# Performance work log

Measured on AMD Instinct MI355X. Metric: run time of the kernel, lower is better.

## Reference

```python
import jax, jax.numpy as jnp
import numpy as np
from jax import lax


def _pw(x, w, b):
    # pointwise conv1d (kernel_size=1) on [B,C,L]
    return jnp.einsum('oc,bcl->bol', w, x) + b[None, :, None]


def _conv(x, w, b, stride):
    y = lax.conv_general_dilated(x, w, (stride,), 'VALID',
                                 dimension_numbers=('NCH', 'OIH', 'NCH'))
    return y + b[None, :, None]


def setup_inputs() -> dict:
    key = jax.random.key(0)
    ks = jax.random.split(key, 40)
    B, L = 512, 300
    d = {}
    d['x'] = jax.random.randint(ks[0], (B, L), 0, 23)
    def w(k, shape, s=0.1):
        return jax.random.normal(k, shape, dtype=jnp.float32) * s
    d['emb'] = w(ks[1], (23, 128), 1.0)
    d['dr_w'] = w(ks[2], (64, 128)); d['dr_b'] = w(ks[3], (64,), 0.01)
    d['c1_w'] = w(ks[4], (64, 64)); d['c1_b'] = w(ks[5], (64,), 0.01)
    d['c11_w'] = w(ks[6], (64, 64)); d['c11_b'] = w(ks[7], (64,), 0.01)
    d['c12_w'] = w(ks[8], (64, 64)); d['c12_b'] = w(ks[9], (64,), 0.01)
    d['c21_w'] = w(ks[10], (64, 64)); d['c21_b'] = w(ks[11], (64,), 0.01)
    d['c22_w'] = w(ks[12], (64, 64)); d['c22_b'] = w(ks[13], (64,), 0.01)
    d['c31_w'] = w(ks[14], (64, 64)); d['c31_b'] = w(ks[15], (64,), 0.01)
    d['c32_w'] = w(ks[16], (64, 64)); d['c32_b'] = w(ks[17], (64,), 0.01)
    d['c41_w'] = w(ks[18], (64, 64)); d['c41_b'] = w(ks[19], (64,), 0.01)
    d['fc_w'] = w(ks[20], (64, 320)); d['fc_b'] = w(ks[21], (64,), 0.01)
    d['cp1_w'] = w(ks[22], (64, 64, 4)); d['cp1_b'] = w(ks[23], (64,), 0.01)
    d['cp2_w'] = w(ks[24], (64, 64, 5)); d['cp2_b'] = w(ks[25], (64,), 0.01)
    d['wt'] = w(ks[26], (64, 64)); d['wx'] = w(ks[27], (64, 64))
    d['bh'] = w(ks[28], (64,), 0.01)
    d['wa'] = w(ks[29], (64,)); d['ba'] = w(ks[30], (1,), 0.01)
    d['m1_w'] = w(ks[31], (100, 960)); d['m1_b'] = w(ks[32], (100,), 0.01)
    d['m2_w'] = w(ks[33], (1, 100)); d['m2_b'] = w(ks[34], (1,), 0.01)
    return d


def reference(x, emb, dr_w, dr_b, c1_w, c1_b, c11_w, c11_b, c12_w, c12_b,
              c21_w, c21_b, c22_w, c22_b, c31_w, c31_b, c32_w, c32_b,
              c41_w, c41_b, fc_w, fc_b, cp1_w, cp1_b, cp2_w, cp2_b,
              wt, wx, bh, wa, ba, m1_w, m1_b, m2_w, m2_b):
    h = emb[x]                                  # [B,L,128]
    h = jnp.transpose(h, (0, 2, 1))             # [B,128,L]
    r = _pw(h, dr_w, dr_b)                      # [B,64,L]
    r = _pw(r, c1_w, c1_b)
    x2 = _pw(_pw(r, c11_w, c11_b), c12_w, c12_b)
    x3 = _pw(_pw(r, c21_w, c21_b), c22_w, c22_b)
    x4 = _pw(_pw(r, c31_w, c31_b), c32_w, c32_b)
    # MaxPool1d(k=3, s=1, p=1)
    xp = jnp.pad(r, ((0, 0), (0, 0), (1, 1)), constant_values=-jnp.inf)
    p = jnp.maximum(jnp.maximum(xp[:, :, :-2], xp[:, :, 1:-1]), xp[:, :, 2:])
    x5 = _pw(p, c41_w, c41_b)
    h = jnp.concatenate([r, x2, x3, x4, x5], axis=1)   # [B,320,L]
    h = _pw(h, fc_w, fc_b)                             # [B,64,L]
    h = _conv(h, cp1_w, cp1_b, 4)                      # [B,64,75]
    a_in = jnp.transpose(h, (0, 2, 1))                 # [B,75,64]
    # additive attention emission
    qt = a_in @ wt.T                                   # Wt(inputs)
    kx = a_in @ wx.T                                   # Wx(inputs)
    hsc = jnp.tanh(qt[:, :, None, :] + kx[:, None, :, :] + bh)  # [B,75,75,64]
    e = jnp.einsum('bijd,d->bij', hsc, wa) + ba[0]     # [B,75,75]
    a = jax.nn.softmax(e, axis=-1)
    v = jnp.einsum('bij,bjd->bid', a, a_in)            # [B,75,64]
    h = jnp.transpose(v, (0, 2, 1))                    # [B,64,75]
    h = jax.nn.relu(h)
    h = _conv(h, cp2_w, cp2_b, 5)                      # [B,64,15]
    h = h.reshape(h.shape[0], -1)                      # [B,960]
    h = jax.nn.relu(h @ m1_w.T + m1_b)
    return h @ m2_w.T + m2_b                           # [B,1]
```

## Files before the change

kernel.cpp:

```cpp
#include <hip/hip_runtime.h>
#include <hip/hip_bf16.h>

#define DEV __device__ __forceinline__

DEV float fexp2(float x) {
#if __has_builtin(__builtin_amdgcn_exp2f)
  return __builtin_amdgcn_exp2f(x);
#else
  return exp2f(x);
#endif
}
DEV float frcp(float x) {
#if __has_builtin(__builtin_amdgcn_rcpf)
  return __builtin_amdgcn_rcpf(x);
#else
  return 1.0f / x;
#endif
}

#define K_C2LOG2E 2.8853900817779268f

__global__ void __launch_bounds__(256)
prep1(const float* __restrict__ emb,
      const float* __restrict__ dr_w, const float* __restrict__ dr_b,
      const float* __restrict__ c1_w, const float* __restrict__ c1_b,
      const float* __restrict__ w11, const float* __restrict__ b11,
      const float* __restrict__ w12, const float* __restrict__ b12,
      const float* __restrict__ w21, const float* __restrict__ b21,
      const float* __restrict__ w22, const float* __restrict__ b22,
      const float* __restrict__ w31, const float* __restrict__ b31,
      const float* __restrict__ w32, const float* __restrict__ b32,
      const float* __restrict__ fc_w, const float* __restrict__ fc_b,
      const float* __restrict__ c41_w, const float* __restrict__ c41_b,
      float* __restrict__ rt_ext, float* __restrict__ T4,
      float* __restrict__ W5, float* __restrict__ bias_fc)
{
  const int v = blockIdx.x, tid = threadIdx.x;
  if (v < 23) {
    __shared__ float A[64], Rt[64], X2[3][64];
    const int c = tid & 63;
    if (tid < 64) {
      float acc = dr_b[c];
      #pragma unroll 8
      for (int e = 0; e < 32; ++e) {
        const float4 wv = *(const float4*)&dr_w[c * 128 + 4 * e];
        const float4 ev = *(const float4*)&emb[v * 128 + 4 * e];
        acc = fmaf(wv.x, ev.x, acc); acc = fmaf(wv.y, ev.y, acc);
        acc = fmaf(wv.z, ev.z, acc); acc = fmaf(wv.w, ev.w, acc);
      }
      A[c] = acc;
    }
    __syncthreads();
    if (tid < 64) {
      float acc = c1_b[c];
      for (int m = 0; m < 64; ++m) acc = fmaf(c1_w[c * 64 + m], A[m], acc);
      Rt[c] = acc;
      rt_ext[v * 64 + c] = acc;
    }
    for (int br = 0; br < 3; ++br) {
      const float* w1 = (br == 0) ? w11 : (br == 1) ? w21 : w31;
      const float* b1 = (br == 0) ? b11 : (br == 1) ? b21 : b31;
      const float* w2 = (br == 0) ? w12 : (br == 1) ? w22 : w32;
      const float* b2 = (br == 0) ? b12 : (br == 1) ? b22 : b32;
      __syncthreads();
      if (tid < 64) {
        float acc = b1[c];
        for (int m = 0; m < 64; ++m) acc = fmaf(w1[c * 64 + m], Rt[m], acc);
        A[c] = acc;
      }
      __syncthreads();
      if (tid < 64) {
        float acc = b2[c];
        for (int m = 0; m < 64; ++m) acc = fmaf(w2[c * 64 + m], A[m], acc);
        X2[br][c] = acc;
      }
    }
    __syncthreads();
    if (tid < 64) {
      float acc = 0.f;
      for (int m = 0; m < 64; ++m) acc = fmaf(fc_w[c * 320 + m],       Rt[m],    acc);
      for (int m = 0; m < 64; ++m) acc = fmaf(fc_w[c * 320 + 64 + m],  X2[0][m], acc);
      for (int m = 0; m < 64; ++m) acc = fmaf(fc_w[c * 320 + 128 + m], X2[1][m], acc);
      for (int m = 0; m < 64; ++m) acc = fmaf(fc_w[c * 320 + 192 + m], X2[2][m], acc);
      T4[v * 64 + c] = acc;
    }
  } else {
    if (tid < 64) rt_ext[23 * 64 + tid] = -1e30f;
    const int m = tid & 63, c0 = (tid >> 6) * 16;
    float acc[16];
    #pragma unroll
    for (int r = 0; r < 16; ++r) acc[r] = 0.f;
    for (int q = 0; q < 64; ++q) {
      const float w = c41_w[q * 64 + m];
      #pragma unroll
      for (int r = 0; r < 16; ++r)
        acc[r] = fmaf(fc_w[(c0 + r) * 320 + 256 + q], w, acc[r]);
    }
    #pragma unroll
    for (int r = 0; r < 16; ++r) W5[(c0 + r) * 64 + m] = acc[r];
    if (tid < 64) {
      float a2 = fc_b[tid];
      for (int q = 0; q < 64; ++q) a2 = fmaf(fc_w[tid * 320 + 256 + q], c41_b[q], a2);
      bias_fc[tid] = a2;
    }
  }
}

__global__ void tab_T5G(const float* __restrict__ cp1_w, const float* __restrict__ cp1_b,
                        const float* __restrict__ T4, const float* __restrict__ W5,
                        const float* __restrict__ bias_fc,
                        float* __restrict__ T5, float* __restrict__ G, float* __restrict__ bb)
{
  const int idx = blockIdx.x * 256 + threadIdx.x;
  if (idx < 5888) {
    const int v = idx >> 8, r = idx & 255, k = r >> 6, o = r & 63;
    float acc = 0.f;
    for (int c = 0; c < 64; ++c) acc = fmaf(cp1_w[o * 256 + c * 4 + k], T4[v * 64 + c], acc);
    T5[v * 256 + k * 64 + o] = acc;
  } else if (idx < 5888 + 16384) {
    const int j = idx - 5888;
    const int k = j >> 12, m = (j >> 6) & 63, o = j & 63;
    float acc = 0.f;
    for (int c = 0; c < 64; ++c) acc = fmaf(cp1_w[o * 256 + c * 4 + k], W5[c * 64 + m], acc);
    G[k * 4096 + m * 64 + o] = acc;
  } else if (idx < 22336) {
    const int o = idx - 22272;
    float acc = cp1_b[o];
    for (int c = 0; c < 64; ++c) {
      float wsum = cp1_w[o * 256 + c * 4 + 0] + cp1_w[o * 256 + c * 4 + 1]
                 + cp1_w[o * 256 + c * 4 + 2] + cp1_w[o * 256 + c * 4 + 3];
      acc = fmaf(wsum, bias_fc[c], acc);
    }
    bb[o] = acc;
  }
}

__global__ void __launch_bounds__(256)
tab_FP5(const float* __restrict__ G, const float* __restrict__ rt_ext,
        float* __restrict__ FP5)
{
  __shared__ float Gl[2][64][64];
  __shared__ float rtl[24 * 64];
  const int tid = threadIdx.x, lane = tid & 63, wave = tid >> 6;
  const int h = blockIdx.x & 1;
  const int vbase = (blockIdx.x >> 1) * 32;
  for (int i = tid; i < 1536; i += 256) rtl[i] = rt_ext[i];
  for (int i = tid; i < 8192; i += 256) ((float*)Gl)[i] = G[h * 8192 + i];
  __syncthreads();
  for (int g = 0; g < 2; ++g) {
    const int j0 = vbase + wave * 8 + g * 4;
    float p[4];
    #pragma unroll
    for (int r = 0; r < 4; ++r) {
      const int v = j0 + r;
      const int a = v / 576, rem = v - a * 576, c = rem / 24, dd = rem - c * 24;
      p[r] = fmaxf(fmaxf(rtl[a * 64 + lane], rtl[c * 64 + lane]), rtl[dd * 64 + lane]);
    }
    float acc[4][2];
    #pragma unroll
    for (int r = 0; r < 4; ++r) { acc[r][0] = 0.f; acc[r][1] = 0.f; }
    #pragma unroll
    for (int m = 0; m < 64; ++m) {
      const float g0 = Gl[0][m][lane], g1 = Gl[1][m][lane];
      #pragma unroll
      for (int r = 0; r < 4; ++r) {
        const float pv = __shfl(p[r], m);
        acc[r][0] = fmaf(g0, pv, acc[r][0]);
        acc[r][1] = fmaf(g1, pv, acc[r][1]);
      }
    }
    #pragma unroll
    for (int r = 0; r < 4; ++r) {
      const int v = j0 + r;
      FP5[v * 256 + (2 * h + 0) * 64 + lane] = acc[r][0];
      FP5[v * 256 + (2 * h + 1) * 64 + lane] = acc[r][1];
    }
  }
}

__global__ void __launch_bounds__(512)
k_main(const int* __restrict__ x,
       const float* __restrict__ wt, const float* __restrict__ wx,
       const float* __restrict__ bh, const float* __restrict__ wa,
       const float* __restrict__ T5, const float* __restrict__ FP5,
       const float* __restrict__ bb, float* __restrict__ vv)
{
  __shared__ int x_lds[304];
  __shared__ __align__(16) float a_in_lds[75 * 64];
  __shared__ __align__(16) float qt_lds[75 * 68];
  __shared__ __align__(16) float kx_lds[75 * 65];
  __shared__ __align__(16) float tail_lds[75 * 12];
  __shared__ float wa_lds[64];

  const int tid = threadIdx.x, lane = tid & 63, wave = tid >> 6;
  const int b = blockIdx.x;

  for (int i = tid; i < 300; i += 512) x_lds[i] = x[b * 300 + i];
  if (tid < 64) wa_lds[tid] = wa[tid];
  __syncthreads();

  {
    const float bbv = bb[lane];
    for (int t = wave; t < 75; t += 8) {
      float acc = bbv;
      #pragma unroll
      for (int k = 0; k < 4; ++k) {
        const int l = 4 * t + k;
        const int xa = (l == 0) ? 23 : x_lds[l - 1];
        const int xd = (l == 299) ? 23 : x_lds[l + 1];
        const int trip = (xa * 576 + x_lds[l] * 24 + xd) * 256;
        acc += T5[x_lds[l] * 256 + k * 64 + lane];
        acc += FP5[trip + k * 64 + lane];
      }
      a_in_lds[t * 64 + lane] = acc;
    }
  }
  __syncthreads();

  {
    float qacc[10];
    #pragma unroll
    for (int r = 0; r < 10; ++r) qacc[r] = 0.f;
    for (int c = 0; c < 4; ++c) {
      const float4 w0 = *(const float4*)&wt[lane * 64 + 16 * c];
      const float4 w1 = *(const float4*)&wt[lane * 64 + 16 * c + 4];
      const float4 w2 = *(const float4*)&wt[lane * 64 + 16 * c + 8];
      const float4 w3 = *(const float4*)&wt[lane * 64 + 16 * c + 12];
      #pragma unroll
      for (int r = 0; r < 10; ++r) {
        const int i = wave + 8 * r;
        if (i < 75) {
          const float* arow = &a_in_lds[i * 64 + 16 * c];
          const float4 a0 = *(const float4*)&arow[0];
          const float4 a1 = *(const float4*)&arow[4];
          const float4 a2 = *(const float4*)&arow[8];
          const float4 a3 = *(const float4*)&arow[12];
          float acc = qacc[r];
          acc = fmaf(w0.x, a0.x, acc); acc = fmaf(w0.y, a0.y, acc);
          acc = fmaf(w0.z, a0.z, acc); acc = fmaf(w0.w, a0.w, acc);
          acc = fmaf(w1.x, a1.x, acc); acc = fmaf(w1.y, a1.y, acc);
          acc = fmaf(w1.z, a1.z, acc); acc = fmaf(w1.w, a1.w, acc);
          acc = fmaf(w2.x, a2.x, acc); acc = fmaf(w2.y, a2.y, acc);
          acc = fmaf(w2.z, a2.z, acc); acc = fmaf(w2.w, a2.w, acc);
          acc = fmaf(w3.x, a3.x, acc); acc = fmaf(w3.y, a3.y, acc);
          acc = fmaf(w3.z, a3.z, acc); acc = fmaf(w3.w, a3.w, acc);
          qacc[r] = acc;
        }
      }
    }
    const float bhv = bh[lane];
    #pragma unroll
    for (int r = 0; r < 10; ++r) {
      const int i = wave + 8 * r;
      if (i < 75) qt_lds[i * 68 + lane] = (qacc[r] + bhv) * K_C2LOG2E;
    }

    #pragma unroll
    for (int r = 0; r < 10; ++r) qacc[r] = 0.f;
    for (int c = 0; c < 4; ++c) {
      const float4 w0 = *(const float4*)&wx[lane * 64 + 16 * c];
      const float4 w1 = *(const float4*)&wx[lane * 64 + 16 * c + 4];
      const float4 w2 = *(const float4*)&wx[lane * 64 + 16 * c + 8];
      const float4 w3 = *(const float4*)&wx[lane * 64 + 16 * c + 12];
      #pragma unroll
      for (int r = 0; r < 10; ++r) {
        const int i = wave + 8 * r;
        if (i < 75) {
          const float* arow = &a_in_lds[i * 64 + 16 * c];
          const float4 a0 = *(const float4*)&arow[0];
          const float4 a1 = *(const float4*)&arow[4];
          const float4 a2 = *(const float4*)&arow[8];
          const float4 a3 = *(const float4*)&arow[12];
          float acc = qacc[r];
          acc = fmaf(w0.x, a0.x, acc); acc = fmaf(w0.y, a0.y, acc);
          acc = fmaf(w0.z, a0.z, acc); acc = fmaf(w0.w, a0.w, acc);
          acc = fmaf(w1.x, a1.x, acc); acc = fmaf(w1.y, a1.y, acc);
          acc = fmaf(w1.z, a1.z, acc); acc = fmaf(w1.w, a1.w, acc);
          acc = fmaf(w2.x, a2.x, acc); acc = fmaf(w2.y, a2.y, acc);
          acc = fmaf(w2.z, a2.z, acc); acc = fmaf(w2.w, a2.w, acc);
          acc = fmaf(w3.x, a3.x, acc); acc = fmaf(w3.y, a3.y, acc);
          acc = fmaf(w3.z, a3.z, acc); acc = fmaf(w3.w, a3.w, acc);
          qacc[r] = acc;
        }
      }
    }
    #pragma unroll
    for (int r = 0; r < 10; ++r) {
      const int i = wave + 8 * r;
      if (i < 75) kx_lds[i * 65 + lane] = qacc[r] * K_C2LOG2E;
    }
  }
  __syncthreads();

  for (int idx = tid; idx < 825; idx += 512) {
    const int i = idx / 11, jt = idx - i * 11;
    const float* qrow = &qt_lds[i * 68];
    const float* krow = &kx_lds[(64 + jt) * 65];
    float S = 0.f;
    #pragma unroll 8
    for (int dd = 0; dd < 64; ++dd) {
      const int d = (dd + lane) & 63;
      const float r = frcp(1.f + fexp2(qrow[d] + krow[d]));
      S = fmaf(wa_lds[d], r, S);
    }
    tail_lds[i * 12 + jt] = S;
  }
  __syncthreads();

  for (int i = wave; i < 75; i += 8) {
    const float* krow = &kx_lds[lane * 65];
    float S1 = 0.f;
    #pragma unroll
    for (int q = 0; q < 16; ++q) {
      const float4 q4 = *(const float4*)&qt_lds[i * 68 + 4 * q];
      const float4 w4 = *(const float4*)&wa_lds[4 * q];
      float r;
      r = frcp(1.f + fexp2(q4.x + krow[4 * q + 0])); S1 = fmaf(w4.x, r, S1);
      r = frcp(1.f + fexp2(q4.y + krow[4 * q + 1])); S1 = fmaf(w4.y, r, S1);
      r = frcp(1.f + fexp2(q4.z + krow[4 * q + 2])); S1 = fmaf(w4.z, r, S1);
      r = frcp(1.f + fexp2(q4.w + krow[4 * q + 3])); S1 = fmaf(w4.w, r, S1);
    }
    const float z1 = S1 * (-K_C2LOG2E);
    const float zt = (lane < 11) ? tail_lds[i * 12 + lane] * (-K_C2LOG2E) : -1e30f;
    float m = fmaxf(z1, zt);
    #pragma unroll
    for (int off = 32; off; off >>= 1) m = fmaxf(m, __shfl_xor(m, off));
    const float p1 = fexp2(z1 - m);
    const float p2 = (lane < 11) ? fexp2(zt - m) : 0.f;
    float s = p1 + p2;
    #pragma unroll
    for (int off = 32; off; off >>= 1) s += __shfl_xor(s, off);
    const float inv = frcp(s);
    const float a1 = p1 * inv, a2 = p2 * inv;

    float acc = 0.f;
    #pragma unroll
    for (int jj = 0; jj < 64; ++jj)
      acc = fmaf(__shfl(a1, jj), a_in_lds[jj * 64 + lane], acc);
    #pragma unroll
    for (int jj = 0; jj < 11; ++jj)
      acc = fmaf(__shfl(a2, jj), a_in_lds[(64 + jj) * 64 + lane], acc);
    vv[b * 4800 + i * 64 + lane] = fmaxf(acc, 0.f);
  }
}

__global__ void __launch_bounds__(256)
k_tail(const float* __restrict__ vv,
       const float* __restrict__ cp2_w, const float* __restrict__ cp2_b,
       const float* __restrict__ m1_w, const float* __restrict__ m1_b,
       const float* __restrict__ m2_w, const float* __restrict__ m2_b,
       float* __restrict__ out)
{
  __shared__ __align__(16) float vv_lds[75 * 65];
  __shared__ float g_lds[2][960];
  __shared__ float y_lds[2][100];
  const int tid = threadIdx.x, lane = tid & 63, wave = tid >> 6;
  const int b0 = blockIdx.x * 2;

  for (int q = 0; q < 2; ++q) {
    const int b = b0 + q;
    __syncthreads();
    for (int idx = tid; idx < 4800; idx += 256) {
      const int i = idx >> 6, d = idx & 63;
      vv_lds[i * 65 + d] = vv[b * 4800 + idx];
    }
    __syncthreads();
    for (int idx = tid; idx < 960; idx += 256) {
      const int o = idx / 15, s = idx % 15;
      float acc = cp2_b[o];
      for (int c = 0; c < 64; ++c) {
        const float* wrow = &cp2_w[(o * 64 + c) * 5];
        const float* vrow = &vv_lds[5 * s * 65 + c];
        #pragma unroll
        for (int k = 0; k < 5; ++k)
          acc = fmaf(wrow[k], vrow[k * 65], acc);
      }
      g_lds[q][idx] = acc;
    }
  }
  __syncthreads();

  for (int u = wave; u < 100; u += 4) {
    float acc0 = 0.f, acc1 = 0.f;
    #pragma unroll
    for (int it = 0; it < 15; ++it) {
      const int n = it * 64 + lane;
      const float w = m1_w[u * 960 + n];
      acc0 = fmaf(w, g_lds[0][n], acc0);
      acc1 = fmaf(w, g_lds[1][n], acc1);
    }
    #pragma unroll
    for (int off = 32; off; off >>= 1) {
      acc0 += __shfl_xor(acc0, off);
      acc1 += __shfl_xor(acc1, off);
    }
    if (lane == 0) {
      const float mb = m1_b[u];
      y_lds[0][u] = fmaxf(acc0 + mb, 0.f);
      y_lds[1][u] = fmaxf(acc1 + mb, 0.f);
    }
  }
  __syncthreads();
  if (wave < 2) {
    const int q = wave;
    float s = y_lds[q][lane] * m2_w[lane];
    if (lane < 36) s = fmaf(y_lds[q][lane + 64], m2_w[lane + 64], s);
    #pragma unroll
    for (int off = 32; off; off >>= 1) s += __shfl_xor(s, off);
    if (lane == 0) out[b0 + q] = s + m2_b[0];
  }
}

extern "C" void kernel_launch(void* const* d_in, const int* in_sizes, int n_in,
                              void* d_out, int out_size, void* d_ws, size_t ws_size,
                              hipStream_t stream) {
  (void)in_sizes; (void)n_in; (void)out_size; (void)ws_size;
  const int*   x     = (const int*)  d_in[0];
  const float* emb   = (const float*)d_in[1];
  const float* dr_w  = (const float*)d_in[2];
  const float* dr_b  = (const float*)d_in[3];
  const float* c1_w  = (const float*)d_in[4];
  const float* c1_b  = (const float*)d_in[5];
  const float* c11_w = (const float*)d_in[6];
  const float* c11_b = (const float*)d_in[7];
  const float* c12_w = (const float*)d_in[8];
  const float* c12_b = (const float*)d_in[9];
  const float* c21_w = (const float*)d_in[10];
  const float* c21_b = (const float*)d_in[11];
  const float* c22_w = (const float*)d_in[12];
  const float* c22_b = (const float*)d_in[13];
  const float* c31_w = (const float*)d_in[14];
  const float* c31_b = (const float*)d_in[15];
  const float* c32_w = (const float*)d_in[16];
  const float* c32_b = (const float*)d_in[17];
  const float* c41_w = (const float*)d_in[18];
  const float* c41_b = (const float*)d_in[19];
  const float* fc_w  = (const float*)d_in[20];
  const float* fc_b  = (const float*)d_in[21];
  const float* cp1_w = (const float*)d_in[22];
  const float* cp1_b = (const float*)d_in[23];
  const float* cp2_w = (const float*)d_in[24];
  const float* cp2_b = (const float*)d_in[25];
  const float* wt    = (const float*)d_in[26];
  const float* wx    = (const float*)d_in[27];
  const float* bh    = (const float*)d_in[28];
  const float* wa    = (const float*)d_in[29];
  const float* m1_w  = (const float*)d_in[31];
  const float* m1_b  = (const float*)d_in[32];
  const float* m2_w  = (const float*)d_in[33];
  const float* m2_b  = (const float*)d_in[34];
  float* out = (float*)d_out;

  float* ws      = (float*)d_ws;
  float* rt_ext  = ws;
  float* T5      = ws + 1536;
  float* bb      = ws + 7424;
  float* G       = ws + 7488;
  float* bias_fc = ws + 23872;
  float* T4      = ws + 28352;
  float* W5      = ws + 29824;
  float* FP5     = ws + 33920;
  float* vv      = ws + 3572864;

  prep1  <<<24, 256, 0, stream>>>(emb, dr_w, dr_b, c1_w, c1_b,
                                  c11_w, c11_b, c12_w, c12_b,
                                  c21_w, c21_b, c22_w, c22_b,
                                  c31_w, c31_b, c32_w, c32_b,
                                  fc_w, fc_b, c41_w, c41_b,
                                  rt_ext, T4, W5, bias_fc);
  tab_T5G<<<88, 256, 0, stream>>>(cp1_w, cp1_b, T4, W5, bias_fc, T5, G, bb);
  tab_FP5<<<864, 256, 0, stream>>>(G, rt_ext, FP5);
  k_main <<<512, 512, 0, stream>>>(x, wt, wx, bh, wa, T5, FP5, bb, vv);
  k_tail <<<256, 256, 0, stream>>>(vv, cp2_w, cp2_b, m1_w, m1_b, m2_w, m2_b, out);
}
```

Measured before the change: 384.3 us.

## Batch attention rows per wave, fuse Q/K projections, restructure table and tail kernels

New measurement: 385.6 us. No clear change (+0.3%).

```diff
diff --git a/kernel.cpp b/kernel.cpp
--- a/kernel.cpp
+++ b/kernel.cpp
@@ -15,6 +15,13 @@
   return __builtin_amdgcn_rcpf(x);
 #else
   return 1.0f / x;
+#endif
+}
+DEV float rdlanef(float v, int l) {
+#if __has_builtin(__builtin_amdgcn_readlane)
+  return __uint_as_float(__builtin_amdgcn_readlane(__float_as_uint(v), l));
+#else
+  return __shfl(v, l);
 #endif
 }
 
@@ -106,32 +113,47 @@
   }
 }
 
-__global__ void tab_T5G(const float* __restrict__ cp1_w, const float* __restrict__ cp1_b,
-                        const float* __restrict__ T4, const float* __restrict__ W5,
-                        const float* __restrict__ bias_fc,
-                        float* __restrict__ T5, float* __restrict__ G, float* __restrict__ bb)
+__global__ void __launch_bounds__(256)
+tab_T5G(const float* __restrict__ cp1_w, const float* __restrict__ cp1_b,
+        const float* __restrict__ T4, const float* __restrict__ W5,
+        const float* __restrict__ bias_fc,
+        float* __restrict__ T5, float* __restrict__ G, float* __restrict__ bb)
 {
-  const int idx = blockIdx.x * 256 + threadIdx.x;
-  if (idx < 5888) {
-    const int v = idx >> 8, r = idx & 255, k = r >> 6, o = r & 63;
-    float acc = 0.f;
-    for (int c = 0; c < 64; ++c) acc = fmaf(cp1_w[o * 256 + c * 4 + k], T4[v * 64 + c], acc);
-    T5[v * 256 + k * 64 + o] = acc;
-  } else if (idx < 5888 + 16384) {
-    const int j = idx - 5888;
-    const int k = j >> 12, m = (j >> 6) & 63, o = j & 63;
-    float acc = 0.f;
-    for (int c = 0; c < 64; ++c) acc = fmaf(cp1_w[o * 256 + c * 4 + k], W5[c * 64 + m], acc);
-    G[k * 4096 + m * 64 + o] = acc;
-  } else if (idx < 22336) {
-    const int o = idx - 22272;
-    float acc = cp1_b[o];
-    for (int c = 0; c < 64; ++c) {
-      float wsum = cp1_w[o * 256 + c * 4 + 0] + cp1_w[o * 256 + c * 4 + 1]
-                 + cp1_w[o * 256 + c * 4 + 2] + cp1_w[o * 256 + c * 4 + 3];
-      acc = fmaf(wsum, bias_fc[c], acc);
-    }
-    bb[o] = acc;
+  const int k = blockIdx.x, tid = threadIdx.x;
+  if (k < 4) {
+    __shared__ float slice[64 * 65];
+    __shared__ float W5l[64 * 64];
+    __shared__ float T4l[23 * 64];
+    for (int i = tid; i < 4096; i += 256) {
+      const int o = i >> 6, c = i & 63;
+      slice[c * 65 + o] = cp1_w[o * 256 + c * 4 + k];
+    }
+    for (int i = tid; i < 4096; i += 256) W5l[i] = W5[i];
+    for (int i = tid; i < 1472; i += 256) T4l[i] = T4[i];
+    __syncthreads();
+    for (int i = tid; i < 1472; i += 256) {
+      const int v = i >> 6, o = i & 63;
+      float acc = 0.f;
+      for (int c = 0; c < 64; ++c)
+        acc = fmaf(slice[c * 65 + o], T4l[v * 64 + c], acc);
+      T5[v * 256 + k * 64 + o] = acc;
+    }
+    for (int i = tid; i < 4096; i += 256) {
+      const int m = i >> 6, o = i & 63;
+      float acc = 0.f;
+      for (int c = 0; c < 64; ++c)
+        acc = fmaf(slice[c * 65 + o], W5l[c * 64 + m], acc);
+      G[k * 4096 + m * 64 + o] = acc;
+    }
+  } else {
+    if (tid < 64) {
+      float acc = cp1_b[tid];
+      for (int c = 0; c < 64; ++c) {
+        const float* p = &cp1_w[tid * 256 + c * 4];
+        acc = fmaf(p[0] + p[1] + p[2] + p[3], bias_fc[c], acc);
+      }
+      bb[tid] = acc;
+    }
   }
 }
 
@@ -218,14 +240,18 @@
   __syncthreads();
 
   {
-    float qacc[10];
-    #pragma unroll
-    for (int r = 0; r < 10; ++r) qacc[r] = 0.f;
+    float qacc[10], kacc[10];
+    #pragma unroll
+    for (int r = 0; r < 10; ++r) { qacc[r] = 0.f; kacc[r] = 0.f; }
     for (int c = 0; c < 4; ++c) {
-      const float4 w0 = *(const float4*)&wt[lane * 64 + 16 * c];
-      const float4 w1 = *(const float4*)&wt[lane * 64 + 16 * c + 4];
-      const float4 w2 = *(const float4*)&wt[lane * 64 + 16 * c + 8];
-      const float4 w3 = *(const float4*)&wt[lane * 64 + 16 * c + 12];
+      const float4 t0 = *(const float4*)&wt[lane * 64 + 16 * c];
+      const float4 t1 = *(const float4*)&wt[lane * 64 + 16 * c + 4];
+      const float4 t2 = *(const float4*)&wt[lane * 64 + 16 * c + 8];
+      const float4 t3 = *(const float4*)&wt[lane * 64 + 16 * c + 12];
+      const float4 x0 = *(const float4*)&wx[lane * 64 + 16 * c];
+      const float4 x1 = *(const float4*)&wx[lane * 64 + 16 * c + 4];
+      const float4 x2 = *(const float4*)&wx[lane * 64 + 16 * c + 8];
+      const float4 x3 = *(const float4*)&wx[lane * 64 + 16 * c + 12];
       #pragma unroll
       for (int r = 0; r < 10; ++r) {
         const int i = wave + 8 * r;
@@ -235,16 +261,24 @@
           const float4 a1 = *(const float4*)&arow[4];
           const float4 a2 = *(const float4*)&arow[8];
           const float4 a3 = *(const float4*)&arow[12];
-          float acc = qacc[r];
-          acc = fmaf(w0.x, a0.x, acc); acc = fmaf(w0.y, a0.y, acc);
-          acc = fmaf(w0.z, a0.z, acc); acc = fmaf(w0.w, a0.w, acc);
-          acc = fmaf(w1.x, a1.x, acc); acc = fmaf(w1.y, a1.y, acc);
-          acc = fmaf(w1.z, a1.z, acc); acc = fmaf(w1.w, a1.w, acc);
-          acc = fmaf(w2.x, a2.x, acc); acc = fmaf(w2.y, a2.y, acc);
-          acc = fmaf(w2.z, a2.z, acc); acc = fmaf(w2.w, a2.w, acc);
-          acc = fmaf(w3.x, a3.x, acc); acc = fmaf(w3.y, a3.y, acc);
-          acc = fmaf(w3.z, a3.z, acc); acc = fmaf(w3.w, a3.w, acc);
-          qacc[r] = acc;
+          float q = qacc[r], kk = kacc[r];
+          q = fmaf(t0.x, a0.x, q); q = fmaf(t0.y, a0.y, q);
+          q = fmaf(t0.z, a0.z, q); q = fmaf(t0.w, a0.w, q);
+          q = fmaf(t1.x, a1.x, q); q = fmaf(t1.y, a1.y, q);
+          q = fmaf(t1.z, a1.z, q); q = fmaf(t1.w, a1.w, q);
+          q = fmaf(t2.x, a2.x, q); q = fmaf(t2.y, a2.y, q);
+          q = fmaf(t2.z, a2.z, q); q = fmaf(t2.w, a2.w, q);
+          q = fmaf(t3.x, a3.x, q); q = fmaf(t3.y, a3.y, q);
+          q = fmaf(t3.z, a3.z, q); q = fmaf(t3.w, a3.w, q);
+          kk = fmaf(x0.x, a0.x, kk); kk = fmaf(x0.y, a0.y, kk);
+          kk = fmaf(x0.z, a0.z, kk); kk = fmaf(x0.w, a0.w, kk);
+          kk = fmaf(x1.x, a1.x, kk); kk = fmaf(x1.y, a1.y, kk);
+          kk = fmaf(x1.z, a1.z, kk); kk = fmaf(x1.w, a1.w, kk);
+          kk = fmaf(x2.x, a2.x, kk); kk = fmaf(x2.y, a2.y, kk);
+          kk = fmaf(x2.z, a2.z, kk); kk = fmaf(x2.w, a2.w, kk);
+          kk = fmaf(x3.x, a3.x, kk); kk = fmaf(x3.y, a3.y, kk);
+          kk = fmaf(x3.z, a3.z, kk); kk = fmaf(x3.w, a3.w, kk);
+          qacc[r] = q; kacc[r] = kk;
         }
       }
     }
@@ -252,42 +286,10 @@
     #pragma unroll
     for (int r = 0; r < 10; ++r) {
       const int i = wave + 8 * r;
-      if (i < 75) qt_lds[i * 68 + lane] = (qacc[r] + bhv) * K_C2LOG2E;
-    }
-
-    #pragma unroll
-    for (int r = 0; r < 10; ++r) qacc[r] = 0.f;
-    for (int c = 0; c < 4; ++c) {
-      const float4 w0 = *(const float4*)&wx[lane * 64 + 16 * c];
-      const float4 w1 = *(const float4*)&wx[lane * 64 + 16 * c + 4];
-      const float4 w2 = *(const float4*)&wx[lane * 64 + 16 * c + 8];
-      const float4 w3 = *(const float4*)&wx[lane * 64 + 16 * c + 12];
-      #pragma unroll
-      for (int r = 0; r < 10; ++r) {
-        const int i = wave + 8 * r;
-        if (i < 75) {
-          const float* arow = &a_in_lds[i * 64 + 16 * c];
-          const float4 a0 = *(const float4*)&arow[0];
-          const float4 a1 = *(const float4*)&arow[4];
-          const float4 a2 = *(const float4*)&arow[8];
-          const float4 a3 = *(const float4*)&arow[12];
-          float acc = qacc[r];
-          acc = fmaf(w0.x, a0.x, acc); acc = fmaf(w0.y, a0.y, acc);
-          acc = fmaf(w0.z, a0.z, acc); acc = fmaf(w0.w, a0.w, acc);
-          acc = fmaf(w1.x, a1.x, acc); acc = fmaf(w1.y, a1.y, acc);
-          acc = fmaf(w1.z, a1.z, acc); acc = fmaf(w1.w, a1.w, acc);
-          acc = fmaf(w2.x, a2.x, acc); acc = fmaf(w2.y, a2.y, acc);
-          acc = fmaf(w2.z, a2.z, acc); acc = fmaf(w2.w, a2.w, acc);
-          acc = fmaf(w3.x, a3.x, acc); acc = fmaf(w3.y, a3.y, acc);
-          acc = fmaf(w3.z, a3.z, acc); acc = fmaf(w3.w, a3.w, acc);
-          qacc[r] = acc;
-        }
-      }
-    }
-    #pragma unroll
-    for (int r = 0; r < 10; ++r) {
-      const int i = wave + 8 * r;
-      if (i < 75) kx_lds[i * 65 + lane] = qacc[r] * K_C2LOG2E;
+      if (i < 75) {
+        qt_lds[i * 68 + lane] = (qacc[r] + bhv) * K_C2LOG2E;
+        kx_lds[i * 65 + lane] = kacc[r] * K_C2LOG2E;
+      }
     }
   }
   __syncthreads();
@@ -307,40 +309,64 @@
   }
   __syncthreads();
 
-  for (int i = wave; i < 75; i += 8) {
+  float a1r[10], a2r[10];
+  #pragma unroll
+  for (int r = 0; r < 10; ++r) { a1r[r] = 0.f; a2r[r] = 0.f; }
+  {
     const float* krow = &kx_lds[lane * 65];
-    float S1 = 0.f;
-    #pragma unroll
-    for (int q = 0; q < 16; ++q) {
-      const float4 q4 = *(const float4*)&qt_lds[i * 68 + 4 * q];
-      const float4 w4 = *(const float4*)&wa_lds[4 * q];
-      float r;
-      r = frcp(1.f + fexp2(q4.x + krow[4 * q + 0])); S1 = fmaf(w4.x, r, S1);
-      r = frcp(1.f + fexp2(q4.y + krow[4 * q + 1])); S1 = fmaf(w4.y, r, S1);
-      r = frcp(1.f + fexp2(q4.z + krow[4 * q + 2])); S1 = fmaf(w4.z, r, S1);
-      r = frcp(1.f + fexp2(q4.w + krow[4 * q + 3])); S1 = fmaf(w4.w, r, S1);
-    }
-    const float z1 = S1 * (-K_C2LOG2E);
-    const float zt = (lane < 11) ? tail_lds[i * 12 + lane] * (-K_C2LOG2E) : -1e30f;
-    float m = fmaxf(z1, zt);
-    #pragma unroll
-    for (int off = 32; off; off >>= 1) m = fmaxf(m, __shfl_xor(m, off));
-    const float p1 = fexp2(z1 - m);
-    const float p2 = (lane < 11) ? fexp2(zt - m) : 0.f;
-    float s = p1 + p2;
-    #pragma unroll
-    for (int off = 32; off; off >>= 1) s += __shfl_xor(s, off);
-    const float inv = frcp(s);
-    const float a1 = p1 * inv, a2 = p2 * inv;
-
-    float acc = 0.f;
-    #pragma unroll
-    for (int jj = 0; jj < 64; ++jj)
-      acc = fmaf(__shfl(a1, jj), a_in_lds[jj * 64 + lane], acc);
-    #pragma unroll
-    for (int jj = 0; jj < 11; ++jj)
-      acc = fmaf(__shfl(a2, jj), a_in_lds[(64 + jj) * 64 + lane], acc);
-    vv[b * 4800 + i * 64 + lane] = fmaxf(acc, 0.f);
+    #pragma unroll
+    for (int r = 0; r < 10; ++r) {
+      const int i = wave + 8 * r;
+      if (i < 75) {
+        float S1 = 0.f;
+        #pragma unroll
+        for (int q = 0; q < 16; ++q) {
+          const float4 q4 = *(const float4*)&qt_lds[i * 68 + 4 * q];
+          const float4 w4 = *(const float4*)&wa_lds[4 * q];
+          float rr;
+          rr = frcp(1.f + fexp2(q4.x + krow[4 * q + 0])); S1 = fmaf(w4.x, rr, S1);
+          rr = frcp(1.f + fexp2(q4.y + krow[4 * q + 1])); S1 = fmaf(w4.y, rr, S1);
+          rr = frcp(1.f + fexp2(q4.z + krow[4 * q + 2])); S1 = fmaf(w4.z, rr, S1);
+          rr = frcp(1.f + fexp2(q4.w + krow[4 * q + 3])); S1 = fmaf(w4.w, rr, S1);
+        }
+        const float z1 = S1 * (-K_C2LOG2E);
+        const float zt = (lane < 11) ? tail_lds[i * 12 + lane] * (-K_C2LOG2E) : -1e30f;
+        float m = fmaxf(z1, zt);
+        #pragma unroll
+        for (int off = 32; off; off >>= 1) m = fmaxf(m, __shfl_xor(m, off));
+        const float p1 = fexp2(z1 - m);
+        const float p2 = (lane < 11) ? fexp2(zt - m) : 0.f;
+        float s = p1 + p2;
+        #pragma unroll
+        for (int off = 32; off; off >>= 1) s += __shfl_xor(s, off);
+        const float inv = frcp(s);
+        a1r[r] = p1 * inv;
+        a2r[r] = p2 * inv;
+      }
+    }
+  }
+
+  {
+    float acc[10];
+    #pragma unroll
+    for (int r = 0; r < 10; ++r) acc[r] = 0.f;
+    for (int j = 0; j < 64; ++j) {
+      const float ajo = a_in_lds[j * 64 + lane];
+      #pragma unroll
+      for (int r = 0; r < 10; ++r)
+        acc[r] = fmaf(rdlanef(a1r[r], j), ajo, acc[r]);
+    }
+    for (int j = 0; j < 11; ++j) {
+      const float ajo = a_in_lds[(64 + j) * 64 + lane];
+      #pragma unroll
+      for (int r = 0; r < 10; ++r)
+        acc[r] = fmaf(rdlanef(a2r[r], j), ajo, acc[r]);
+    }
+    #pragma unroll
+    for (int r = 0; r < 10; ++r) {
+      const int i = wave + 8 * r;
+      if (i < 75) vv[b * 4800 + i * 64 + lane] = fmaxf(acc[r], 0.f);
+    }
   }
 }
 
@@ -352,62 +378,48 @@
        float* __restrict__ out)
 {
   __shared__ __align__(16) float vv_lds[75 * 65];
-  __shared__ float g_lds[2][960];
-  __shared__ float y_lds[2][100];
+  __shared__ float g_lds[960];
+  __shared__ float y_lds[100];
   const int tid = threadIdx.x, lane = tid & 63, wave = tid >> 6;
-  const int b0 = blockIdx.x * 2;
-
-  for (int q = 0; q < 2; ++q) {
-    const int b = b0 + q;
-    __syncthreads();
-    for (int idx = tid; idx < 4800; idx += 256) {
-      const int i = idx >> 6, d = idx & 63;
-      vv_lds[i * 65 + d] = vv[b * 4800 + idx];
-    }
-    __syncthreads();
-    for (int idx = tid; idx < 960; idx += 256) {
-      const int o = idx / 15, s = idx % 15;
-      float acc = cp2_b[o];
-      for (int c = 0; c < 64; ++c) {
-        const float* wrow = &cp2_w[(o * 64 + c) * 5];
-        const float* vrow = &vv_lds[5 * s * 65 + c];
-        #pragma unroll
-        for (int k = 0; k < 5; ++k)
-          acc = fmaf(wrow[k], vrow[k * 65], acc);
-      }
-      g_lds[q][idx] = acc;
-    }
+  const int b = blockIdx.x;
+
+  for (int idx = tid; idx < 4800; idx += 256) {
+    const int i = idx >> 6, d = idx & 63;
+    vv_lds[i * 65 + d] = vv[b * 4800 + idx];
+  }
+  __syncthreads();
+  for (int idx = tid; idx < 960; idx += 256) {
+    const int s = idx >> 6, o = idx & 63;
+    float acc = cp2_b[o];
+    for (int c = 0; c < 64; ++c) {
+      const float* wrow = &cp2_w[(o * 64 + c) * 5];
+      const float* vrow = &vv_lds[5 * s * 65 + c];
+      #pragma unroll
+      for (int k = 0; k < 5; ++k)
+        acc = fmaf(wrow[k], vrow[k * 65], acc);
+    }
+    g_lds[o * 15 + s] = acc;
   }
   __syncthreads();
 
   for (int u = wave; u < 100; u += 4) {
-    float acc0 = 0.f, acc1 = 0.f;
+    float acc0 = 0.f;
     #pragma unroll
     for (int it = 0; it < 15; ++it) {
       const int n = it * 64 + lane;
-      const float w = m1_w[u * 960 + n];
-      acc0 = fmaf(w, g_lds[0][n], acc0);
-      acc1 = fmaf(w, g_lds[1][n], acc1);
-    }
-    #pragma unroll
-    for (int off = 32; off; off >>= 1) {
-      acc0 += __shfl_xor(acc0, off);
-      acc1 += __shfl_xor(acc1, off);
-    }
-    if (lane == 0) {
-      const float mb = m1_b[u];
-      y_lds[0][u] = fmaxf(acc0 + mb, 0.f);
-      y_lds[1][u] = fmaxf(acc1 + mb, 0.f);
-    }
-  }
-  __syncthreads();
-  if (wave < 2) {
-    const int q = wave;
-    float s = y_lds[q][lane] * m2_w[lane];
-    if (lane < 36) s = fmaf(y_lds[q][lane + 64], m2_w[lane + 64], s);
+      acc0 = fmaf(m1_w[u * 960 + n], g_lds[n], acc0);
+    }
+    #pragma unroll
+    for (int off = 32; off; off >>= 1) acc0 += __shfl_xor(acc0, off);
+    if (lane == 0) y_lds[u] = fmaxf(acc0 + m1_b[u], 0.f);
+  }
+  __syncthreads();
+  if (wave == 0) {
+    float s = y_lds[lane] * m2_w[lane];
+    if (lane < 36) s = fmaf(y_lds[lane + 64], m2_w[lane + 64], s);
     #pragma unroll
     for (int off = 32; off; off >>= 1) s += __shfl_xor(s, off);
-    if (lane == 0) out[b0 + q] = s + m2_b[0];
+    if (lane == 0) out[b] = s + m2_b[0];
   }
 }
 
@@ -468,8 +480,8 @@
                                   c31_w, c31_b, c32_w, c32_b,
                                   fc_w, fc_b, c41_w, c41_b,
                                   rt_ext, T4, W5, bias_fc);
-  tab_T5G<<<88, 256, 0, stream>>>(cp1_w, cp1_b, T4, W5, bias_fc, T5, G, bb);
+  tab_T5G<<<5, 256, 0, stream>>>(cp1_w, cp1_b, T4, W5, bias_fc, T5, G, bb);
   tab_FP5<<<864, 256, 0, stream>>>(G, rt_ext, FP5);
   k_main <<<512, 512, 0, stream>>>(x, wt, wx, bh, wa, T5, FP5, bb, vv);
-  k_tail <<<256, 256, 0, stream>>>(vv, cp2_w, cp2_b, m1_w, m1_b, m2_w, m2_b, out);
-}
+  k_tail <<<512, 256, 0, stream>>>(vv, cp2_w, cp2_b, m1_w, m1_b, m2_w, m2_b, out);
+}
```
